# Optimization experiments

Measured on AMD Instinct MI355X. Metric: run time of the kernel, lower is better.

Reference implementation:

```python
import jax, jax.numpy as jnp
import numpy as np

TYPE_NUM = 4
NUM_INPUTS = 128
BATCH = 4096
NODE_NUM = 256
HID = 16


def _xavier_uniform(key, shape, gain=1.414):
    fan_in, fan_out = shape[-2], shape[-1]
    lim = gain * (6.0 / (fan_in + fan_out)) ** 0.5
    return jax.random.uniform(key, shape, jnp.float32, -lim, lim)


def setup_inputs() -> dict:
    key = jax.random.key(0)
    k0, k1, k2, k3, k4 = jax.random.split(key, 5)
    x = jax.random.normal(k0, (BATCH, NODE_NUM, NUM_INPUTS), jnp.float32)
    a1 = _xavier_uniform(k1, (TYPE_NUM, 2 * NUM_INPUTS, HID))
    a2 = _xavier_uniform(k2, (TYPE_NUM, HID, 1))
    # binary neighbor mask over nodes; ensure at least one neighbor
    adj_mask = jax.random.randint(k3, (NODE_NUM,), 0, 2).astype(jnp.float32).at[0].set(1.0)
    type_index = jax.random.randint(k4, (BATCH,), 0, TYPE_NUM)
    node_index = 0
    return dict(x=x, a1=a1, a2=a2, adj_mask=adj_mask,
                node_index=node_index, type_index=type_index)


def reference(x, a1, a2, adj_mask, node_index, type_index):
    # x: [B, N, F]; a1: [T, 2F, H]; a2: [T, H, 1]; adj_mask: [N]; type_index: [B]
    B, N, Fdim = x.shape
    T = a1.shape[0]
    tgt = jnp.broadcast_to(x[:, node_index, :][:, None, :], (B, N, Fdim))
    concat = jnp.concatenate([tgt, x], axis=-1)            # [B, N, 2F]
    h = jax.nn.leaky_relu(jnp.einsum('bnc,tch->tbnh', concat, a1))   # [T, B, N, H]
    e = jax.nn.leaky_relu(jnp.einsum('tbnh,th->tbn', h, a2[:, :, 0]))  # [T, B, N]
    neg = jnp.asarray(-9e15, e.dtype)
    att = jnp.where(adj_mask > 0, e, neg)                  # mask broadcasts over [T,B,N]
    att = jax.nn.softmax(att, axis=-1) * adj_mask          # [T, B, N]
    onehot = jax.nn.one_hot(type_index, T, dtype=x.dtype)  # [B, T]
    probs = jnp.einsum('tbn,bt->bn', att, onehot)          # [B, N] -> Categorical probs
    return probs
```

## Files before the change

### kernel.cpp

```cpp
#include <hip/hip_runtime.h>
#include <math.h>

#define BATCH 4096
#define NODES 256
#define FDIM  128
#define HID   16

typedef __attribute__((ext_vector_type(8))) short short8;
typedef __attribute__((ext_vector_type(4))) float f32x4;

__device__ __forceinline__ short bf_rn(float x) {
    const unsigned u = __float_as_uint(x);
    return (short)((u + 0x7FFF + ((u >> 16) & 1)) >> 16);
}
__device__ __forceinline__ float bf_back(short s) {
    return __uint_as_float(((unsigned)(unsigned short)s) << 16);
}
__device__ __forceinline__ void split8(float4 v0, float4 v1,
                                       short8& hi, short8& lo) {
    float v[8] = {v0.x, v0.y, v0.z, v0.w, v1.x, v1.y, v1.z, v1.w};
    #pragma unroll
    for (int j = 0; j < 8; ++j) {
        const short h = bf_rn(v[j]);
        hi[j] = h;
        lo[j] = bf_rn(v[j] - bf_back(h));
    }
}

__launch_bounds__(256)
__global__ void mta_kernel(const float* __restrict__ x,
                           const float* __restrict__ a1,
                           const float* __restrict__ a2,
                           const float* __restrict__ adj,
                           const int*  __restrict__ node_index,
                           const int*  __restrict__ type_index,
                           float* __restrict__ out) {
    const int tid  = threadIdx.x;
    const int lane = tid & 63;
    const int w    = tid >> 6;
    const int b    = blockIdx.x * 4 + w;
    const int n    = lane & 15;
    const int g    = lane >> 4;

    __shared__ float es[4][NODES];

    const int t  = __builtin_amdgcn_readfirstlane(type_index[b]);
    const int ni = __builtin_amdgcn_readfirstlane(node_index[0]);

    const float* At  = a1 + (size_t)t * (2 * FDIM * HID);
    const float* Ab  = At + FDIM * HID;
    const float* a2t = a2 + t * HID;
    const float* xb  = x + (size_t)b * NODES * FDIM;

    float c0 = 0.f;
    {
        const float* x0  = xb + (size_t)ni * FDIM + g * 32;
        const float* Atg = At + (g * 32) * HID + n;
        #pragma unroll
        for (int j4 = 0; j4 < 8; ++j4) {
            const float4 xv = *(const float4*)(x0 + j4 * 4);
            c0 = fmaf(xv.x, Atg[(j4 * 4 + 0) * HID], c0);
            c0 = fmaf(xv.y, Atg[(j4 * 4 + 1) * HID], c0);
            c0 = fmaf(xv.z, Atg[(j4 * 4 + 2) * HID], c0);
            c0 = fmaf(xv.w, Atg[(j4 * 4 + 3) * HID], c0);
        }
        c0 += __shfl_xor(c0, 16);
        c0 += __shfl_xor(c0, 32);
    }

    short8 wfrag[4];
    #pragma unroll
    for (int kt = 0; kt < 4; ++kt) {
        #pragma unroll
        for (int j = 0; j < 8; ++j)
            wfrag[kt][j] = bf_rn(Ab[(kt * 32 + g * 8 + j) * HID + n]);
    }
    const float a2h = a2t[n];

    float* esw = es[w];
    #pragma unroll 1
    for (int mt = 0; mt < 16; ++mt) {
        float4 ra[4][2];
        #pragma unroll
        for (int kt = 0; kt < 4; ++kt) {
            const float* p = xb + (size_t)(mt * 16 + n) * FDIM
                           + kt * 32 + g * 8;
            ra[kt][0] = *(const float4*)p;
            ra[kt][1] = *(const float4*)(p + 4);
        }
        f32x4 acc = (f32x4){0.f, 0.f, 0.f, 0.f};
        #pragma unroll
        for (int kt = 0; kt < 4; ++kt) {
            short8 ahi, alo;
            split8(ra[kt][0], ra[kt][1], ahi, alo);
            acc = __builtin_amdgcn_mfma_f32_16x16x32_bf16(ahi, wfrag[kt], acc, 0, 0, 0);
            acc = __builtin_amdgcn_mfma_f32_16x16x32_bf16(alo, wfrag[kt], acc, 0, 0, 0);
        }
        #pragma unroll
        for (int r = 0; r < 4; ++r) {
            float v = acc[r] + c0;
            v = (v > 0.f) ? v : 0.01f * v;
            float s = v * a2h;
            s += __shfl_xor(s, 1);
            s += __shfl_xor(s, 2);
            s += __shfl_xor(s, 4);
            s += __shfl_xor(s, 8);
            const float e = (s > 0.f) ? s : 0.01f * s;
            if (n == 0) esw[mt * 16 + g * 4 + r] = e;
        }
    }

    const float4 ev = *(const float4*)&esw[lane * 4];
    const float4 mv = *(const float4*)&adj[lane * 4];
    const float NEG = -INFINITY;
    float e0 = (mv.x > 0.f) ? ev.x : NEG;
    float e1 = (mv.y > 0.f) ? ev.y : NEG;
    float e2 = (mv.z > 0.f) ? ev.z : NEG;
    float e3 = (mv.w > 0.f) ? ev.w : NEG;

    float mx = fmaxf(fmaxf(e0, e1), fmaxf(e2, e3));
    #pragma unroll
    for (int off = 32; off; off >>= 1) mx = fmaxf(mx, __shfl_xor(mx, off));

    const float p0 = (mv.x > 0.f) ? __expf(e0 - mx) : 0.f;
    const float p1 = (mv.y > 0.f) ? __expf(e1 - mx) : 0.f;
    const float p2 = (mv.z > 0.f) ? __expf(e2 - mx) : 0.f;
    const float p3 = (mv.w > 0.f) ? __expf(e3 - mx) : 0.f;

    float s = (p0 + p1) + (p2 + p3);
    #pragma unroll
    for (int off = 32; off; off >>= 1) s += __shfl_xor(s, off);
    const float rz = 1.f / s;

    float4 ov = {p0 * rz, p1 * rz, p2 * rz, p3 * rz};
    *(float4*)&out[(size_t)b * NODES + lane * 4] = ov;
}

extern "C" void kernel_launch(void* const* d_in, const int* in_sizes, int n_in,
                              void* d_out, int out_size, void* d_ws, size_t ws_size,
                              hipStream_t stream) {
    const float* x   = (const float*)d_in[0];
    const float* a1  = (const float*)d_in[1];
    const float* a2  = (const float*)d_in[2];
    const float* adj = (const float*)d_in[3];
    const int*   ni  = (const int*)d_in[4];
    const int*   ti  = (const int*)d_in[5];
    float* out = (float*)d_out;

    mta_kernel<<<BATCH / 4, 256, 0, stream>>>(x, a1, a2, adj, ni, ti, out);
}
```

Measured before the change: 109.0 us.

## Double-buffer x tiles into LDS via async global_load_lds with XOR swizzle

Replaces direct per-lane global float4 loads of each 16-row x tile with async global-to-LDS loads into a per-wave double buffer, prefetching the next tile while the current one is consumed. Reads from LDS use an XOR swizzle to avoid bank conflicts. The aim is to hide global memory latency on this memory-bound kernel, at the cost of 64KB of extra shared memory per block, which lowers occupancy, and of relying on a manual vmcnt wait with no LDS barrier.

```diff
diff --git a/kernel.cpp b/kernel.cpp
--- a/kernel.cpp
+++ b/kernel.cpp
@@ -27,6 +27,12 @@
     }
 }
 
+__device__ __forceinline__ void gload_lds16(const float* g, void* l) {
+    __builtin_amdgcn_global_load_lds(
+        (const __attribute__((address_space(1))) void*)g,
+        (__attribute__((address_space(3))) void*)l, 16, 0, 0);
+}
+
 __launch_bounds__(256)
 __global__ void mta_kernel(const float* __restrict__ x,
                            const float* __restrict__ a1,
@@ -42,6 +48,7 @@
     const int n    = lane & 15;
     const int g    = lane >> 4;
 
+    __shared__ __align__(16) float stg[4][2][16 * FDIM];
     __shared__ float es[4][NODES];
 
     const int t  = __builtin_amdgcn_readfirstlane(type_index[b]);
@@ -76,26 +83,45 @@
             wfrag[kt][j] = bf_rn(Ab[(kt * 32 + g * 8 + j) * HID + n]);
     }
     const float a2h = a2t[n];
+    float* esw = es[w];
 
-    float* esw = es[w];
+    auto stg_tile = [&](int mt, int p) {
+        float* dst = &stg[w][p][0];
+        const float* src = xb + (size_t)mt * 16 * FDIM;
+        #pragma unroll
+        for (int i = 0; i < 8; ++i) {
+            const int s   = i * 64 + lane;
+            const int row = s >> 5;
+            const int c16 = s & 31;
+            gload_lds16(src + row * FDIM + ((c16 ^ (row & 7)) << 2),
+                        (char*)dst + i * 1024);
+        }
+    };
+
+    stg_tile(0, 0);
     #pragma unroll 1
     for (int mt = 0; mt < 16; ++mt) {
-        float4 ra[4][2];
-        #pragma unroll
-        for (int kt = 0; kt < 4; ++kt) {
-            const float* p = xb + (size_t)(mt * 16 + n) * FDIM
-                           + kt * 32 + g * 8;
-            ra[kt][0] = *(const float4*)p;
-            ra[kt][1] = *(const float4*)(p + 4);
+        const int p = mt & 1;
+        if (mt + 1 < 16) {
+            stg_tile(mt + 1, p ^ 1);
+            asm volatile("s_waitcnt vmcnt(8)" ::: "memory");
+        } else {
+            asm volatile("s_waitcnt vmcnt(0)" ::: "memory");
         }
+
+        const char* srcb = (const char*)&stg[w][p][0];
         f32x4 acc = (f32x4){0.f, 0.f, 0.f, 0.f};
         #pragma unroll
         for (int kt = 0; kt < 4; ++kt) {
+            const int ca = kt * 8 + g * 2;
+            const float4 v0 = *(const float4*)(srcb + n * 512 + ((ca ^ (n & 7)) << 4));
+            const float4 v1 = *(const float4*)(srcb + n * 512 + (((ca + 1) ^ (n & 7)) << 4));
             short8 ahi, alo;
-            split8(ra[kt][0], ra[kt][1], ahi, alo);
+            split8(v0, v1, ahi, alo);
             acc = __builtin_amdgcn_mfma_f32_16x16x32_bf16(ahi, wfrag[kt], acc, 0, 0, 0);
             acc = __builtin_amdgcn_mfma_f32_16x16x32_bf16(alo, wfrag[kt], acc, 0, 0, 0);
         }
+
         #pragma unroll
         for (int r = 0; r < 4; ++r) {
             float v = acc[r] + c0;
```

After: 107.9 us. About the same (-1.0%).
